# Performance work log

Measured on AMD Instinct MI355X. Metric: run time of the kernel, lower is better.

The kernel has to match this reference:

```python
import jax, jax.numpy as jnp
import numpy as np

N_NODES = 16000
N_EDGES = 256000
F = 128        # invariant edge feature dim
MUL = 64       # multiplicity of env/V irreps (mul_gcd)
HID = 128      # mlp_n_hidden
SQRT3 = float(np.sqrt(3.0))

# e3nn-style activation normalization constant for silu:
# c = sqrt(E_{z~N(0,1)}[silu(z)^2]), so silu(z)/c has unit second moment.
_z = np.linspace(-12.0, 12.0, 100001)
_pdf = np.exp(-0.5 * _z ** 2) / np.sqrt(2.0 * np.pi)
_silu = _z / (1.0 + np.exp(-_z))
SILU_C = float(np.sqrt(np.trapz(_silu ** 2 * _pdf, _z)))


def _nsilu(x):
    return jax.nn.silu(x) / SILU_C


def _lin(x, W):
    # e3nn 'path' gradient normalization: W ~ N(0,1), forward scaled by 1/sqrt(fan_in)
    return (x @ W) / jnp.sqrt(jnp.asarray(W.shape[0], x.dtype))


def setup_inputs() -> dict:
    key = jax.random.key(0)
    ks = jax.random.split(key, 11)
    inp = {
        'vectors': jax.random.normal(ks[0], (N_EDGES, 3), jnp.float32),
        'x': jax.random.normal(ks[1], (N_EDGES, F), jnp.float32),
        'V': jax.random.normal(ks[2], (N_EDGES, 4 * MUL), jnp.float32),  # 64x0e + 64x1o
        'u': jax.random.uniform(ks[3], (N_EDGES,), jnp.float32),
        'm': jnp.ones((N_EDGES,), jnp.float32),
        'W_env': jax.random.normal(ks[4], (F, 2 * MUL), jnp.float32),
        'W1': jax.random.normal(ks[5], (F + 2 * MUL, HID), jnp.float32),
        'W2': jax.random.normal(ks[6], (HID, HID), jnp.float32),
        'W3': jax.random.normal(ks[7], (HID, HID), jnp.float32),
        'W_out': jax.random.normal(ks[8], (2 * MUL, MUL), jnp.float32),
        'senders': jax.random.randint(ks[9], (N_EDGES,), 0, N_NODES, jnp.int32),
    }
    return inp


def reference(vectors, x, V, u, m, W_env, W1, W2, W3, W_out, senders):
    E = vectors.shape[0]
    x = x * m[:, None]

    # n_neighbors = scatter_sum(m, dst=senders, map_back=True)
    n_neighbors = jax.ops.segment_sum(m, senders, num_segments=N_NODES)[senders]  # (E,)

    # w = Linear(num_irreps=2*MUL)(x)
    w = _lin(x, W_env)                  # (E, 128)
    w0, w1 = w[:, :MUL], w[:, MUL:]     # scalar / vector channel weights

    # spherical harmonics (component normalization): Y0 = 1, Y1 = sqrt(3)*rhat
    rhat = vectors / jnp.linalg.norm(vectors, axis=-1, keepdims=True)
    Y1 = SQRT3 * rhat                   # (E, 3)

    # w * Y * m, scatter_sum over senders, map back, normalize by n_neighbors
    denom = n_neighbors + 1e-5
    ws = w0 * m[:, None]                                   # (E, MUL)   w * Y0
    wv = (w1[:, :, None] * Y1[:, None, :]) * m[:, None, None]  # (E, MUL, 3)
    wY_s = jax.ops.segment_sum(ws, senders, num_segments=N_NODES)[senders] / denom[:, None]
    wY_v = jax.ops.segment_sum(wv, senders, num_segments=N_NODES)[senders] / denom[:, None, None]

    # V.mul_to_axis(): (E, MUL, 0e+1o)
    Vs = V[:, :MUL]                      # (E, MUL)
    Vv = V[:, MUL:].reshape(E, MUL, 3)   # (E, MUL, 3)

    # tensor product, filter_ir_out = {0e, 1o} (CG, component normalization)
    s_a = wY_s * Vs                                  # 0e x 0e -> 0e
    s_b = jnp.sum(wY_v * Vv, axis=-1) / SQRT3        # 1o x 1o -> 0e
    v_a = wY_s[:, :, None] * Vv                      # 0e x 1o -> 1o
    v_b = wY_v * Vs[:, :, None]                      # 1o x 0e -> 1o

    # scalars -> concatenated into x; vectors stay equivariant
    x = jnp.concatenate([x, s_a, s_b], axis=1)       # (E, F + 2*MUL)

    # invariant MLP (silu, no output activation)
    h = _nsilu(_lin(x, W1))
    h = _nsilu(_lin(h, W2))
    h = _lin(h, W3)                                  # (E, HID)
    x_out = u[:, None] * h

    # Linear(irreps_out=64x1o) on 128x1o
    V_in = jnp.concatenate([v_a, v_b], axis=1)       # (E, 2*MUL, 3)
    V_out = jnp.einsum('euk,uo->eok', V_in, W_out) / jnp.sqrt(jnp.asarray(2 * MUL, V.dtype))
    V_out = V_out.reshape(E, MUL * 3)                # (E, 192)

    return x_out, V_out
```

## Files before the change

kernel.cpp:

```cpp
#include <hip/hip_runtime.h>
#include <math.h>

typedef short bf16x8 __attribute__((ext_vector_type(8)));
typedef float f32x4 __attribute__((ext_vector_type(4)));

#define S128 0.08838834764831845f
#define S256I 0.0625f
#define NN_NODES 16000

#define WS_COUNTS   16448000
#define WS_OFFSETS  (WS_COUNTS + 64000)
#define WS_CURSOR   (WS_OFFSETS + 64000)
#define WS_ORDER    (WS_CURSOR + 64000)
#define WS_W1 (WS_ORDER + 1024000)
#define WS_W2 (WS_W1 + 65536)
#define WS_W3 (WS_W2 + 32768)
#define WS_WO (WS_W3 + 32768)
#define WS_WE (WS_WO + 16384)

static float compute_inv_silu_c() {
    double sum = 0.0, prev = 0.0;
    const double dz = 24.0 / 100000.0;
    for (int i = 0; i <= 100000; ++i) {
        double z = -12.0 + dz * (double)i;
        double pdf = exp(-0.5 * z * z) * 0.3989422804014327;
        double s = z / (1.0 + exp(-z));
        double f = s * s * pdf;
        if (i) sum += 0.5 * (prev + f) * dz;
        prev = f;
    }
    return (float)(1.0 / sqrt(sum));
}
static const float INV_SILU_C = compute_inv_silu_c();

__device__ __forceinline__ unsigned int packbf(float a, float b) {
    union { float f; unsigned int u; } ca, cb;
    ca.f = a; cb.f = b;
    unsigned int ua = ca.u + (0x7fffu + ((ca.u >> 16) & 1u));
    unsigned int ub = cb.u + (0x7fffu + ((cb.u >> 16) & 1u));
    return (ua >> 16) | (ub & 0xffff0000u);
}
__device__ __forceinline__ unsigned short bf16r(float v) {
    union { float f; unsigned int u; } c; c.f = v;
    return (unsigned short)((c.u + (0x7fffu + ((c.u >> 16) & 1u))) >> 16);
}
__device__ __forceinline__ float bflo(unsigned int u) { return __uint_as_float(u << 16); }
__device__ __forceinline__ float bfhi(unsigned int u) { return __uint_as_float(u & 0xffff0000u); }
__device__ __forceinline__ int swz(int row, int b) { return b ^ ((row & 7) << 4); }
__device__ __forceinline__ float nsilu(float v, float ic) {
    return v / (1.0f + __expf(-v)) * ic;
}

__global__ __launch_bounds__(256) void k_wprep(
    const float* __restrict__ W1, const float* __restrict__ W2,
    const float* __restrict__ W3, const float* __restrict__ Wout,
    const float* __restrict__ Wenv, char* __restrict__ wsb)
{
    const int t = blockIdx.x * 256 + threadIdx.x;
    if (t < NN_NODES) ((int*)(wsb + WS_COUNTS))[t] = 0;
    if (t < 32768) {
        int n = t & 127, k = t >> 7;
        *(unsigned short*)(wsb + WS_W1 + n * 512 + k * 2) =
            bf16r(W1[k * 128 + n] * S256I);
    }
    if (t < 16384) {
        int n = t & 127, k = t >> 7;
        *(unsigned short*)(wsb + WS_W2 + n * 256 + k * 2) =
            bf16r(W2[k * 128 + n] * S128);
        *(unsigned short*)(wsb + WS_W3 + n * 256 + k * 2) =
            bf16r(W3[k * 128 + n] * S128);
    }
    if (t < 16384) {
        int j = t & 127, k = t >> 7;
        int c = (j & 1) ? 64 + (j >> 1) : (j >> 1);
        *(unsigned short*)(wsb + WS_WE + j * 256 + ((k * 2) ^ ((j & 7) << 4))) =
            bf16r(Wenv[k * 128 + c] * S128);
    }
    if (t < 8192) {
        int o = t & 63, uu = t >> 6;
        *(unsigned short*)(wsb + WS_WO + o * 256 + ((uu * 2) ^ ((o & 7) << 4))) =
            bf16r(Wout[uu * 64 + o] * S128);
    }
}

__global__ __launch_bounds__(1024) void k_hist(
    const int* __restrict__ senders, int* __restrict__ counts, int E)
{
    const int e = blockIdx.x * 1024 + threadIdx.x;
    if (e < E) atomicAdd(&counts[senders[e]], 1);
}

__global__ __launch_bounds__(1024) void k_scan(
    const int* __restrict__ counts, int* __restrict__ offsets,
    int* __restrict__ cursor)
{
    __shared__ int part[1024];
    const int t = threadIdx.x;
    const int s0 = t * 16;
    const int s1 = (s0 + 16 < NN_NODES) ? s0 + 16 : NN_NODES;
    int s = 0;
    for (int i = s0; i < s1; ++i) s += counts[i];
    part[t] = s;
    __syncthreads();
    for (int off = 1; off < 1024; off <<= 1) {
        int v = part[t];
        if (t >= off) v += part[t - off];
        __syncthreads();
        part[t] = v;
        __syncthreads();
    }
    int run = t ? part[t - 1] : 0;
    for (int i = s0; i < s1; ++i) {
        offsets[i] = run; cursor[i] = run; run += counts[i];
    }
}

__global__ __launch_bounds__(1024) void k_binfill(
    const int* __restrict__ senders, int* __restrict__ cursor,
    int* __restrict__ order, int E)
{
    const int e = blockIdx.x * 1024 + threadIdx.x;
    if (e < E) {
        const int p = atomicAdd(&cursor[senders[e]], 1);
        order[p] = e;
    }
}

__global__ __launch_bounds__(512) void k_env(
    const float* __restrict__ x, const float* __restrict__ m,
    const char* __restrict__ wsb, char* __restrict__ wout, int E)
{
    __shared__ char lds[65536];
    const int tid = threadIdx.x;

    {
        const int4* src = (const int4*)(wsb + WS_WE);
        int4* dst = (int4*)(lds + 32768);
        #pragma unroll
        for (int j = 0; j < 4; ++j) dst[tid * 4 + j] = src[tid * 4 + j];
    }

    const int eb = blockIdx.x * 128;
    {
        const int el = tid >> 2, q = tid & 3;
        const int e = eb + el;
        if (e < E) {
            const float mv = m[e];
            const float4* xp = (const float4*)&x[(size_t)e * 128 + q * 32];
            #pragma unroll
            for (int j = 0; j < 4; ++j) {
                float4 A = xp[2 * j], B = xp[2 * j + 1];
                int4 w;
                w.x = packbf(A.x * mv, A.y * mv); w.y = packbf(A.z * mv, A.w * mv);
                w.z = packbf(B.x * mv, B.y * mv); w.w = packbf(B.z * mv, B.w * mv);
                *(int4*)(lds + el * 256 + swz(el, q * 64 + j * 16)) = w;
            }
        } else {
            const int4 z = {0, 0, 0, 0};
            #pragma unroll
            for (int j = 0; j < 4; ++j)
                *(int4*)(lds + el * 256 + swz(el, q * 64 + j * 16)) = z;
        }
    }
    __syncthreads();

    const int l = tid & 63, wid = tid >> 6;
    const int wm = wid & 3, wn = wid >> 2;
    const int m0 = wm * 32, n0 = wn * 64;
    const int lr = l & 15, lg = l >> 4;

    f32x4 acc[2][4];
    #pragma unroll
    for (int a = 0; a < 2; ++a)
        #pragma unroll
        for (int b = 0; b < 4; ++b) acc[a][b] = (f32x4){0.f, 0.f, 0.f, 0.f};

    #pragma unroll
    for (int kk = 0; kk < 4; ++kk) {
        const int kb = kk * 64 + lg * 16;
        bf16x8 a0 = *(const bf16x8*)(lds + (m0 + lr) * 256      + swz(m0 + lr, kb));
        bf16x8 a1 = *(const bf16x8*)(lds + (m0 + 16 + lr) * 256 + swz(m0 + 16 + lr, kb));
        #pragma unroll
        for (int nt = 0; nt < 4; ++nt) {
            const int row = n0 + nt * 16 + lr;
            bf16x8 bb = *(const bf16x8*)(lds + 32768 + row * 256 + swz(row, kb));
            acc[0][nt] = __builtin_amdgcn_mfma_f32_16x16x32_bf16(a0, bb, acc[0][nt], 0, 0, 0);
            acc[1][nt] = __builtin_amdgcn_mfma_f32_16x16x32_bf16(a1, bb, acc[1][nt], 0, 0, 0);
        }
    }
    __syncthreads();

    #pragma unroll
    for (int mt = 0; mt < 2; ++mt)
        #pragma unroll
        for (int nt = 0; nt < 4; ++nt)
            #pragma unroll
            for (int r = 0; r < 4; ++r) {
                const int row = m0 + mt * 16 + lg * 4 + r;
                const int col = n0 + nt * 16 + lr;
                *(unsigned short*)(lds + row * 256 + col * 2) = bf16r(acc[mt][nt][r]);
            }
    __syncthreads();
    {
        const int4* s = (const int4*)lds;
        int4* d = (int4*)(wout + (size_t)eb * 256);
        #pragma unroll
        for (int j = 0; j < 4; ++j) d[tid * 4 + j] = s[tid * 4 + j];
    }
}

__global__ __launch_bounds__(256) void k_gather(
    const char* __restrict__ wvb, const float* __restrict__ vectors,
    const float* __restrict__ m, const int* __restrict__ counts,
    const int* __restrict__ offsets, const int* __restrict__ order,
    float* __restrict__ node_cnt, float* __restrict__ node_s,
    float* __restrict__ node_v)
{
    const int l = threadIdx.x & 63, wid = threadIdx.x >> 6;
    const int n = blockIdx.x * 4 + wid;
    if (n >= NN_NODES) return;
    const int cnt = counts[n], base = offsets[n];

    float as = 0.f, a0 = 0.f, a1 = 0.f, a2 = 0.f, am = 0.f;
    for (int i = 0; i < cnt; ++i) {
        const int e = order[base + i];
        const unsigned int wv = *(const unsigned int*)(wvb + (size_t)e * 256 + l * 4);
        const float mm = m[e];
        const float vx = vectors[(size_t)e * 3 + 0];
        const float vy = vectors[(size_t)e * 3 + 1];
        const float vz = vectors[(size_t)e * 3 + 2];
        const float rn = 1.7320508075688772f / sqrtf(vx * vx + vy * vy + vz * vz);
        const float w0 = bflo(wv) * mm;
        const float c1 = bfhi(wv) * mm * rn;
        as += w0; am += mm;
        a0 += c1 * vx; a1 += c1 * vy; a2 += c1 * vz;
    }
    if (l == 0) node_cnt[n] = am;
    node_s[(size_t)n * 64 + l] = as;
    float* nv = &node_v[((size_t)n * 64 + l) * 3];
    nv[0] = a0; nv[1] = a1; nv[2] = a2;
}

__global__ __launch_bounds__(512) void k_prep_vout(
    const float* __restrict__ V, const int* __restrict__ senders,
    const float* __restrict__ node_cnt, const float* __restrict__ node_s,
    const float* __restrict__ node_v, const char* __restrict__ wsb,
    float* __restrict__ out_x, float* __restrict__ out_v, int E)
{
    __shared__ char lds[49152 + 16384];
    const int tid = threadIdx.x, l = tid & 63, wid = tid >> 6;

    {
        const int4* src = (const int4*)(wsb + WS_WO);
        int4 a = src[tid * 2], b = src[tid * 2 + 1];
        ((int4*)(lds + 49152))[tid * 2]     = a;
        ((int4*)(lds + 49152))[tid * 2 + 1] = b;
    }

    const int eb = blockIdx.x * 64;
    #pragma unroll 2
    for (int i = 0; i < 8; ++i) {
        const int el = wid * 8 + i;
        const int e  = eb + el;
        float Vs = 0.f, Vv0 = 0.f, Vv1 = 0.f, Vv2 = 0.f;
        float wYs = 0.f, wv0 = 0.f, wv1 = 0.f, wv2 = 0.f;
        if (e < E) {
            Vs = V[(size_t)e * 256 + l];
            const float* vp = &V[(size_t)e * 256 + 64 + l * 3];
            Vv0 = vp[0]; Vv1 = vp[1]; Vv2 = vp[2];
            const int sn = senders[e];
            const float rden = 1.0f / (node_cnt[sn] + 1e-5f);
            wYs = node_s[(size_t)sn * 64 + l] * rden;
            const float* nvp = &node_v[((size_t)sn * 64 + l) * 3];
            wv0 = nvp[0] * rden; wv1 = nvp[1] * rden; wv2 = nvp[2] * rden;
            unsigned short* sab = (unsigned short*)((char*)out_x + (size_t)e * 512);
            sab[l]      = bf16r(wYs * Vs);
            sab[64 + l] = bf16r((wv0 * Vv0 + wv1 * Vv1 + wv2 * Vv2) * 0.57735026918962576f);
        }
        const float vvk[3] = {Vv0, Vv1, Vv2};
        const float wvk[3] = {wv0, wv1, wv2};
        #pragma unroll
        for (int k = 0; k < 3; ++k) {
            const int row = el * 3 + k;
            *(unsigned short*)(lds + row * 256 + swz(row, l * 2))       = bf16r(wYs * vvk[k]);
            *(unsigned short*)(lds + row * 256 + swz(row, 128 + l * 2)) = bf16r(wvk[k] * Vs);
        }
    }
    __syncthreads();

    const int wm = wid & 3, wn = wid >> 2;
    const int m0 = wm * 48, n0 = wn * 32;
    const int lr = l & 15, lg = l >> 4;
    f32x4 acc[3][2];
    #pragma unroll
    for (int a = 0; a < 3; ++a)
        #pragma unroll
        for (int b = 0; b < 2; ++b) acc[a][b] = (f32x4){0.f, 0.f, 0.f, 0.f};

    #pragma unroll
    for (int kk = 0; kk < 4; ++kk) {
        const int kb = kk * 64 + lg * 16;
        bf16x8 a0 = *(const bf16x8*)(lds + (m0 + lr) * 256      + swz(m0 + lr, kb));
        bf16x8 a1 = *(const bf16x8*)(lds + (m0 + 16 + lr) * 256 + swz(m0 + 16 + lr, kb));
        bf16x8 a2 = *(const bf16x8*)(lds + (m0 + 32 + lr) * 256 + swz(m0 + 32 + lr, kb));
        bf16x8 b0 = *(const bf16x8*)(lds + 49152 + (n0 + lr) * 256      + swz(n0 + lr, kb));
        bf16x8 b1 = *(const bf16x8*)(lds + 49152 + (n0 + 16 + lr) * 256 + swz(n0 + 16 + lr, kb));
        acc[0][0] = __builtin_amdgcn_mfma_f32_16x16x32_bf16(a0, b0, acc[0][0], 0, 0, 0);
        acc[0][1] = __builtin_amdgcn_mfma_f32_16x16x32_bf16(a0, b1, acc[0][1], 0, 0, 0);
        acc[1][0] = __builtin_amdgcn_mfma_f32_16x16x32_bf16(a1, b0, acc[1][0], 0, 0, 0);
        acc[1][1] = __builtin_amdgcn_mfma_f32_16x16x32_bf16(a1, b1, acc[1][1], 0, 0, 0);
        acc[2][0] = __builtin_amdgcn_mfma_f32_16x16x32_bf16(a2, b0, acc[2][0], 0, 0, 0);
        acc[2][1] = __builtin_amdgcn_mfma_f32_16x16x32_bf16(a2, b1, acc[2][1], 0, 0, 0);
    }
    __syncthreads();

    #pragma unroll
    for (int mt = 0; mt < 3; ++mt)
        #pragma unroll
        for (int nt = 0; nt < 2; ++nt)
            #pragma unroll
            for (int r = 0; r < 4; ++r) {
                const int mm = m0 + mt * 16 + lg * 4 + r;
                const int el2 = mm / 3, kd = mm - el2 * 3;
                const int o = n0 + nt * 16 + lr;
                *(float*)(lds + el2 * 768 + (o * 3 + kd) * 4) = acc[mt][nt][r];
            }
    __syncthreads();
    if (eb + 64 <= E) {
        const int4* s = (const int4*)lds;
        int4* d = (int4*)(out_v + (size_t)eb * 192);
        #pragma unroll
        for (int j = 0; j < 6; ++j) d[tid * 6 + j] = s[tid * 6 + j];
    } else {
        for (int idx = tid; idx < 64 * 192; idx += 512) {
            const int el2 = idx / 192;
            if (eb + el2 < E)
                out_v[(size_t)(eb + el2) * 192 + (idx % 192)] = *(float*)(lds + idx * 4);
        }
    }
}

__global__ __launch_bounds__(512, 4) void k_mlp(
    const float* __restrict__ x, const float* __restrict__ m,
    const float* __restrict__ ug, const char* __restrict__ wsb,
    float* __restrict__ out_x, float inv_c, int E)
{
    __shared__ char lds[65536];
    const int tid = threadIdx.x;

    const int eb = blockIdx.x * 128;
    {
        const int el = tid >> 2, q = tid & 3;
        const int e  = eb + el;
        if (e < E) {
            const float mv = m[e];
            const float4* xp = (const float4*)&x[(size_t)e * 128 + q * 32];
            #pragma unroll
            for (int j = 0; j < 4; ++j) {
                float4 A = xp[2 * j], B = xp[2 * j + 1];
                int4 w;
                w.x = packbf(A.x * mv, A.y * mv); w.y = packbf(A.z * mv, A.w * mv);
                w.z = packbf(B.x * mv, B.y * mv); w.w = packbf(B.z * mv, B.w * mv);
                *(int4*)(lds + el * 512 + swz(el, q * 64 + j * 16)) = w;
            }
            const int4* sp = (const int4*)((const char*)out_x + (size_t)e * 512 + q * 64);
            #pragma unroll
            for (int j = 0; j < 4; ++j) {
                int4 v = sp[j];
                *(int4*)(lds + el * 512 + swz(el, 256 + q * 64 + j * 16)) = v;
            }
        } else {
            const int4 z = {0, 0, 0, 0};
            #pragma unroll
            for (int j = 0; j < 4; ++j) {
                *(int4*)(lds + el * 512 + swz(el, q * 64 + j * 16)) = z;
                *(int4*)(lds + el * 512 + swz(el, 256 + q * 64 + j * 16)) = z;
            }
        }
    }
    __syncthreads();

    const int l = tid & 63, wid = tid >> 6;
    const int wm = wid >> 1, wn = wid & 1;
    const int m0 = wm * 32, n0 = wn * 64;
    const int lr = l & 15, lg = l >> 4;

    const char* w1g = wsb + WS_W1;
    const char* w2g = wsb + WS_W2;
    const char* w3g = wsb + WS_W3;

    f32x4 acc[2][4];
    #pragma unroll
    for (int a = 0; a < 2; ++a)
        #pragma unroll
        for (int b = 0; b < 4; ++b) acc[a][b] = (f32x4){0.f, 0.f, 0.f, 0.f};
    #pragma unroll 2
    for (int kk = 0; kk < 8; ++kk) {
        const int kb = kk * 64 + lg * 16;
        bf16x8 a0 = *(const bf16x8*)(lds + (m0 + lr) * 512      + swz(m0 + lr, kb));
        bf16x8 a1 = *(const bf16x8*)(lds + (m0 + 16 + lr) * 512 + swz(m0 + 16 + lr, kb));
        #pragma unroll
        for (int nt = 0; nt < 4; ++nt) {
            const int row = n0 + nt * 16 + lr;
            bf16x8 bb = *(const bf16x8*)(w1g + row * 512 + kb);
            acc[0][nt] = __builtin_amdgcn_mfma_f32_16x16x32_bf16(a0, bb, acc[0][nt], 0, 0, 0);
            acc[1][nt] = __builtin_amdgcn_mfma_f32_16x16x32_bf16(a1, bb, acc[1][nt], 0, 0, 0);
        }
    }
    __syncthreads();

    #pragma unroll
    for (int mt = 0; mt < 2; ++mt)
        #pragma unroll
        for (int nt = 0; nt < 4; ++nt)
            #pragma unroll
            for (int r = 0; r < 4; ++r) {
                const int row = m0 + mt * 16 + lg * 4 + r;
                const int col = n0 + nt * 16 + lr;
                *(unsigned short*)(lds + row * 256 + swz(row, col * 2)) =
                    bf16r(nsilu(acc[mt][nt][r], inv_c));
            }
    __syncthreads();

    f32x4 acc2[2][4];
    #pragma unroll
    for (int a = 0; a < 2; ++a)
        #pragma unroll
        for (int b = 0; b < 4; ++b) acc2[a][b] = (f32x4){0.f, 0.f, 0.f, 0.f};
    #pragma unroll
    for (int kk = 0; kk < 4; ++kk) {
        const int kb = kk * 64 + lg * 16;
        bf16x8 a0 = *(const bf16x8*)(lds + (m0 + lr) * 256      + swz(m0 + lr, kb));
        bf16x8 a1 = *(const bf16x8*)(lds + (m0 + 16 + lr) * 256 + swz(m0 + 16 + lr, kb));
        #pragma unroll
        for (int nt = 0; nt < 4; ++nt) {
            const int row = n0 + nt * 16 + lr;
            bf16x8 bb = *(const bf16x8*)(w2g + row * 256 + kb);
            acc2[0][nt] = __builtin_amdgcn_mfma_f32_16x16x32_bf16(a0, bb, acc2[0][nt], 0, 0, 0);
            acc2[1][nt] = __builtin_amdgcn_mfma_f32_16x16x32_bf16(a1, bb, acc2[1][nt], 0, 0, 0);
        }
    }
    #pragma unroll
    for (int mt = 0; mt < 2; ++mt)
        #pragma unroll
        for (int nt = 0; nt < 4; ++nt)
            #pragma unroll
            for (int r = 0; r < 4; ++r) {
                const int row = m0 + mt * 16 + lg * 4 + r;
                const int col = n0 + nt * 16 + lr;
                *(unsigned short*)(lds + 32768 + row * 256 + swz(row, col * 2)) =
                    bf16r(nsilu(acc2[mt][nt][r], inv_c));
            }
    __syncthreads();

    f32x4 acc3[2][4];
    #pragma unroll
    for (int a = 0; a < 2; ++a)
        #pragma unroll
        for (int b = 0; b < 4; ++b) acc3[a][b] = (f32x4){0.f, 0.f, 0.f, 0.f};
    #pragma unroll
    for (int kk = 0; kk < 4; ++kk) {
        const int kb = kk * 64 + lg * 16;
        bf16x8 a0 = *(const bf16x8*)(lds + 32768 + (m0 + lr) * 256      + swz(m0 + lr, kb));
        bf16x8 a1 = *(const bf16x8*)(lds + 32768 + (m0 + 16 + lr) * 256 + swz(m0 + 16 + lr, kb));
        #pragma unroll
        for (int nt = 0; nt < 4; ++nt) {
            const int row = n0 + nt * 16 + lr;
            bf16x8 bb = *(const bf16x8*)(w3g + row * 256 + kb);
            acc3[0][nt] = __builtin_amdgcn_mfma_f32_16x16x32_bf16(a0, bb, acc3[0][nt], 0, 0, 0);
            acc3[1][nt] = __builtin_amdgcn_mfma_f32_16x16x32_bf16(a1, bb, acc3[1][nt], 0, 0, 0);
        }
    }
    #pragma unroll
    for (int mt = 0; mt < 2; ++mt)
        #pragma unroll
        for (int r = 0; r < 4; ++r) {
            const int e = eb + m0 + mt * 16 + lg * 4 + r;
            if (e < E) {
                const float uu = ug[e];
                #pragma unroll
                for (int nt = 0; nt < 4; ++nt)
                    out_x[(size_t)e * 128 + n0 + nt * 16 + lr] = uu * acc3[mt][nt][r];
            }
        }
}

extern "C" void kernel_launch(void* const* d_in, const int* in_sizes, int n_in,
                              void* d_out, int out_size, void* d_ws, size_t ws_size,
                              hipStream_t stream) {
    const float* vectors = (const float*)d_in[0];
    const float* x       = (const float*)d_in[1];
    const float* V       = (const float*)d_in[2];
    const float* u       = (const float*)d_in[3];
    const float* m       = (const float*)d_in[4];
    const float* W_env   = (const float*)d_in[5];
    const float* W1      = (const float*)d_in[6];
    const float* W2      = (const float*)d_in[7];
    const float* W3      = (const float*)d_in[8];
    const float* W_out   = (const float*)d_in[9];
    const int*   senders = (const int*)d_in[10];

    const int E = in_sizes[4];

    char*  wsb      = (char*)d_ws;
    float* node_cnt = (float*)d_ws;
    float* node_s   = node_cnt + NN_NODES;
    float* node_v   = node_s + (size_t)NN_NODES * 64;
    int* counts  = (int*)(wsb + WS_COUNTS);
    int* offsets = (int*)(wsb + WS_OFFSETS);
    int* cursor  = (int*)(wsb + WS_CURSOR);
    int* order   = (int*)(wsb + WS_ORDER);

    float* out_x = (float*)d_out;
    float* out_v = out_x + (size_t)E * 128;
    char*  wvb   = (char*)out_v;

    k_wprep<<<128, 256, 0, stream>>>(W1, W2, W3, W_out, W_env, wsb);
    k_hist<<<(E + 1023) / 1024, 1024, 0, stream>>>(senders, counts, E);
    k_scan<<<1, 1024, 0, stream>>>(counts, offsets, cursor);
    k_binfill<<<(E + 1023) / 1024, 1024, 0, stream>>>(senders, cursor, order, E);
    k_env<<<(E + 127) / 128, 512, 0, stream>>>(x, m, wsb, wvb, E);
    k_gather<<<(NN_NODES + 3) / 4, 256, 0, stream>>>(wvb, vectors, m, counts,
                                                     offsets, order,
                                                     node_cnt, node_s, node_v);
    k_prep_vout<<<(E + 63) / 64, 512, 0, stream>>>(V, senders, node_cnt, node_s,
                                                   node_v, wsb, out_x, out_v, E);
    k_mlp<<<(E + 127) / 128, 512, 0, stream>>>(x, m, u, wsb, out_x, INV_SILU_C, E);
}
```

Baseline: 507.4 us.

## Hold weight fragments in registers and stage outputs through LDS in env and MLP kernels

```diff
diff --git a/kernel.cpp b/kernel.cpp
--- a/kernel.cpp
+++ b/kernel.cpp
@@ -73,7 +73,7 @@
     if (t < 16384) {
         int j = t & 127, k = t >> 7;
         int c = (j & 1) ? 64 + (j >> 1) : (j >> 1);
-        *(unsigned short*)(wsb + WS_WE + j * 256 + ((k * 2) ^ ((j & 7) << 4))) =
+        *(unsigned short*)(wsb + WS_WE + j * 256 + k * 2) =
             bf16r(Wenv[k * 128 + c] * S128);
     }
     if (t < 8192) {
@@ -130,15 +130,15 @@
     const float* __restrict__ x, const float* __restrict__ m,
     const char* __restrict__ wsb, char* __restrict__ wout, int E)
 {
-    __shared__ char lds[65536];
-    const int tid = threadIdx.x;
-
-    {
-        const int4* src = (const int4*)(wsb + WS_WE);
-        int4* dst = (int4*)(lds + 32768);
-        #pragma unroll
-        for (int j = 0; j < 4; ++j) dst[tid * 4 + j] = src[tid * 4 + j];
-    }
+    __shared__ char lds[32768];
+    const int tid = threadIdx.x, l = tid & 63, wid = tid >> 6;
+    const int lr = l & 15, lg = l >> 4;
+    const int n0 = wid * 16;
+
+    bf16x8 B[4];
+    #pragma unroll
+    for (int kk = 0; kk < 4; ++kk)
+        B[kk] = *(const bf16x8*)(wsb + WS_WE + (n0 + lr) * 256 + kk * 64 + lg * 16);
 
     const int eb = blockIdx.x * 128;
     {
@@ -149,10 +149,10 @@
             const float4* xp = (const float4*)&x[(size_t)e * 128 + q * 32];
             #pragma unroll
             for (int j = 0; j < 4; ++j) {
-                float4 A = xp[2 * j], B = xp[2 * j + 1];
+                float4 A = xp[2 * j], Bv = xp[2 * j + 1];
                 int4 w;
                 w.x = packbf(A.x * mv, A.y * mv); w.y = packbf(A.z * mv, A.w * mv);
-                w.z = packbf(B.x * mv, B.y * mv); w.w = packbf(B.z * mv, B.w * mv);
+                w.z = packbf(Bv.x * mv, Bv.y * mv); w.w = packbf(Bv.z * mv, Bv.w * mv);
                 *(int4*)(lds + el * 256 + swz(el, q * 64 + j * 16)) = w;
             }
         } else {
@@ -164,48 +164,41 @@
     }
     __syncthreads();
 
-    const int l = tid & 63, wid = tid >> 6;
-    const int wm = wid & 3, wn = wid >> 2;
-    const int m0 = wm * 32, n0 = wn * 64;
-    const int lr = l & 15, lg = l >> 4;
-
-    f32x4 acc[2][4];
-    #pragma unroll
-    for (int a = 0; a < 2; ++a)
-        #pragma unroll
-        for (int b = 0; b < 4; ++b) acc[a][b] = (f32x4){0.f, 0.f, 0.f, 0.f};
+    f32x4 acc[8];
+    #pragma unroll
+    for (int a = 0; a < 8; ++a) acc[a] = (f32x4){0.f, 0.f, 0.f, 0.f};
 
     #pragma unroll
     for (int kk = 0; kk < 4; ++kk) {
         const int kb = kk * 64 + lg * 16;
-        bf16x8 a0 = *(const bf16x8*)(lds + (m0 + lr) * 256      + swz(m0 + lr, kb));
-        bf16x8 a1 = *(const bf16x8*)(lds + (m0 + 16 + lr) * 256 + swz(m0 + 16 + lr, kb));
-        #pragma unroll
-        for (int nt = 0; nt < 4; ++nt) {
-            const int row = n0 + nt * 16 + lr;
-            bf16x8 bb = *(const bf16x8*)(lds + 32768 + row * 256 + swz(row, kb));
-            acc[0][nt] = __builtin_amdgcn_mfma_f32_16x16x32_bf16(a0, bb, acc[0][nt], 0, 0, 0);
-            acc[1][nt] = __builtin_amdgcn_mfma_f32_16x16x32_bf16(a1, bb, acc[1][nt], 0, 0, 0);
-        }
-    }
-    __syncthreads();
-
-    #pragma unroll
-    for (int mt = 0; mt < 2; ++mt)
-        #pragma unroll
-        for (int nt = 0; nt < 4; ++nt)
+        #pragma unroll
+        for (int mt = 0; mt < 8; ++mt) {
+            const int row = mt * 16 + lr;
+            bf16x8 a = *(const bf16x8*)(lds + row * 256 + swz(row, kb));
+            acc[mt] = __builtin_amdgcn_mfma_f32_16x16x32_bf16(a, B[kk], acc[mt], 0, 0, 0);
+        }
+    }
+    __syncthreads();
+
+    #pragma unroll
+    for (int mt = 0; mt < 8; ++mt)
+        #pragma unroll
+        for (int r = 0; r < 4; ++r) {
+            const int row = mt * 16 + lg * 4 + r;
+            *(unsigned short*)(lds + row * 256 + (((n0 + lr) * 2) ^ ((row & 7) << 4))) =
+                bf16r(acc[mt][r]);
+        }
+    __syncthreads();
+
+    {
+        const int el = tid >> 2, q = tid & 3;
+        const int e = eb + el;
+        if (e < E) {
+            int4* d = (int4*)(wout + (size_t)e * 256 + q * 64);
             #pragma unroll
-            for (int r = 0; r < 4; ++r) {
-                const int row = m0 + mt * 16 + lg * 4 + r;
-                const int col = n0 + nt * 16 + lr;
-                *(unsigned short*)(lds + row * 256 + col * 2) = bf16r(acc[mt][nt][r]);
-            }
-    __syncthreads();
-    {
-        const int4* s = (const int4*)lds;
-        int4* d = (int4*)(wout + (size_t)eb * 256);
-        #pragma unroll
-        for (int j = 0; j < 4; ++j) d[tid * 4 + j] = s[tid * 4 + j];
+            for (int j = 0; j < 4; ++j)
+                d[j] = *(int4*)(lds + el * 256 + ((q * 64 + j * 16) ^ ((el & 7) << 4)));
+        }
     }
 }
 
@@ -345,144 +338,137 @@
     const float* __restrict__ ug, const char* __restrict__ wsb,
     float* __restrict__ out_x, float inv_c, int E)
 {
-    __shared__ char lds[65536];
-    const int tid = threadIdx.x;
-
-    const int eb = blockIdx.x * 128;
+    __shared__ char lds[49152];
+    const int tid = threadIdx.x, l = tid & 63, wid = tid >> 6;
+    const int lr = l & 15, lg = l >> 4;
+    const int n0 = wid * 16;
+    const int eb = blockIdx.x * 64;
+
+    bf16x8 B1[8];
+    #pragma unroll
+    for (int kk = 0; kk < 8; ++kk)
+        B1[kk] = *(const bf16x8*)(wsb + WS_W1 + (n0 + lr) * 512 + kk * 64 + lg * 16);
+
     {
-        const int el = tid >> 2, q = tid & 3;
-        const int e  = eb + el;
+        const int el = tid >> 3, q = tid & 7;
+        const int e = eb + el;
         if (e < E) {
             const float mv = m[e];
-            const float4* xp = (const float4*)&x[(size_t)e * 128 + q * 32];
+            const float4* xp = (const float4*)&x[(size_t)e * 128 + q * 16];
+            float4 A = xp[0], Bv = xp[1], C = xp[2], D = xp[3];
+            int4 w0, w1;
+            w0.x = packbf(A.x * mv, A.y * mv);   w0.y = packbf(A.z * mv, A.w * mv);
+            w0.z = packbf(Bv.x * mv, Bv.y * mv); w0.w = packbf(Bv.z * mv, Bv.w * mv);
+            w1.x = packbf(C.x * mv, C.y * mv);   w1.y = packbf(C.z * mv, C.w * mv);
+            w1.z = packbf(D.x * mv, D.y * mv);   w1.w = packbf(D.z * mv, D.w * mv);
+            *(int4*)(lds + el * 512 + swz(el, q * 32))      = w0;
+            *(int4*)(lds + el * 512 + swz(el, q * 32 + 16)) = w1;
+            const int4* sp = (const int4*)((const char*)out_x + (size_t)e * 512 + q * 32);
+            *(int4*)(lds + el * 512 + swz(el, 256 + q * 32))      = sp[0];
+            *(int4*)(lds + el * 512 + swz(el, 256 + q * 32 + 16)) = sp[1];
+        } else {
+            const int4 z = {0, 0, 0, 0};
+            *(int4*)(lds + el * 512 + swz(el, q * 32))            = z;
+            *(int4*)(lds + el * 512 + swz(el, q * 32 + 16))       = z;
+            *(int4*)(lds + el * 512 + swz(el, 256 + q * 32))      = z;
+            *(int4*)(lds + el * 512 + swz(el, 256 + q * 32 + 16)) = z;
+        }
+    }
+    __syncthreads();
+
+    f32x4 a1[4];
+    #pragma unroll
+    for (int a = 0; a < 4; ++a) a1[a] = (f32x4){0.f, 0.f, 0.f, 0.f};
+    #pragma unroll
+    for (int kk = 0; kk < 8; ++kk) {
+        const int kb = kk * 64 + lg * 16;
+        #pragma unroll
+        for (int mt = 0; mt < 4; ++mt) {
+            const int row = mt * 16 + lr;
+            bf16x8 a = *(const bf16x8*)(lds + row * 512 + swz(row, kb));
+            a1[mt] = __builtin_amdgcn_mfma_f32_16x16x32_bf16(a, B1[kk], a1[mt], 0, 0, 0);
+        }
+    }
+
+    bf16x8 B2[4], B3[4];
+    #pragma unroll
+    for (int kk = 0; kk < 4; ++kk) {
+        B2[kk] = *(const bf16x8*)(wsb + WS_W2 + (n0 + lr) * 256 + kk * 64 + lg * 16);
+        B3[kk] = *(const bf16x8*)(wsb + WS_W3 + (n0 + lr) * 256 + kk * 64 + lg * 16);
+    }
+
+    #pragma unroll
+    for (int mt = 0; mt < 4; ++mt)
+        #pragma unroll
+        for (int r = 0; r < 4; ++r) {
+            const int row = mt * 16 + lg * 4 + r;
+            *(unsigned short*)(lds + 32768 + row * 256 + swz(row, (n0 + lr) * 2)) =
+                bf16r(nsilu(a1[mt][r], inv_c));
+        }
+    __syncthreads();
+
+    f32x4 a2[4];
+    #pragma unroll
+    for (int a = 0; a < 4; ++a) a2[a] = (f32x4){0.f, 0.f, 0.f, 0.f};
+    #pragma unroll
+    for (int kk = 0; kk < 4; ++kk) {
+        const int kb = kk * 64 + lg * 16;
+        #pragma unroll
+        for (int mt = 0; mt < 4; ++mt) {
+            const int row = mt * 16 + lr;
+            bf16x8 a = *(const bf16x8*)(lds + 32768 + row * 256 + swz(row, kb));
+            a2[mt] = __builtin_amdgcn_mfma_f32_16x16x32_bf16(a, B2[kk], a2[mt], 0, 0, 0);
+        }
+    }
+    #pragma unroll
+    for (int mt = 0; mt < 4; ++mt)
+        #pragma unroll
+        for (int r = 0; r < 4; ++r) {
+            const int row = mt * 16 + lg * 4 + r;
+            *(unsigned short*)(lds + row * 256 + swz(row, (n0 + lr) * 2)) =
+                bf16r(nsilu(a2[mt][r], inv_c));
+        }
+    __syncthreads();
+
+    f32x4 a3[4];
+    #pragma unroll
+    for (int a = 0; a < 4; ++a) a3[a] = (f32x4){0.f, 0.f, 0.f, 0.f};
+    #pragma unroll
+    for (int kk = 0; kk < 4; ++kk) {
+        const int kb = kk * 64 + lg * 16;
+        #pragma unroll
+        for (int mt = 0; mt < 4; ++mt) {
+            const int row = mt * 16 + lr;
+            bf16x8 a = *(const bf16x8*)(lds + row * 256 + swz(row, kb));
+            a3[mt] = __builtin_amdgcn_mfma_f32_16x16x32_bf16(a, B3[kk], a3[mt], 0, 0, 0);
+        }
+    }
+    __syncthreads();
+
+    #pragma unroll
+    for (int mt = 0; mt < 4; ++mt)
+        #pragma unroll
+        for (int r = 0; r < 4; ++r) {
+            const int row = mt * 16 + lg * 4 + r;
+            *(float*)(lds + row * 512 + (((n0 + lr) * 4) ^ ((row & 7) << 4))) = a3[mt][r];
+        }
+    __syncthreads();
+
+    {
+        const int el = tid >> 3, q = tid & 7;
+        const int e = eb + el;
+        if (e < E) {
+            const float uu = ug[e];
             #pragma unroll
             for (int j = 0; j < 4; ++j) {
-                float4 A = xp[2 * j], B = xp[2 * j + 1];
-                int4 w;
-                w.x = packbf(A.x * mv, A.y * mv); w.y = packbf(A.z * mv, A.w * mv);
-                w.z = packbf(B.x * mv, B.y * mv); w.w = packbf(B.z * mv, B.w * mv);
-                *(int4*)(lds + el * 512 + swz(el, q * 64 + j * 16)) = w;
+                int4 v = *(int4*)(lds + el * 512 + ((q * 64 + j * 16) ^ ((el & 7) << 4)));
+                float4 f;
+                f.x = __int_as_float(v.x) * uu; f.y = __int_as_float(v.y) * uu;
+                f.z = __int_as_float(v.z) * uu; f.w = __int_as_float(v.w) * uu;
+                *(float4*)(&out_x[(size_t)e * 128 + q * 16 + j * 4]) = f;
             }
-            const int4* sp = (const int4*)((const char*)out_x + (size_t)e * 512 + q * 64);
-            #pragma unroll
-            for (int j = 0; j < 4; ++j) {
-                int4 v = sp[j];
-                *(int4*)(lds + el * 512 + swz(el, 256 + q * 64 + j * 16)) = v;
-            }
-        } else {
-            const int4 z = {0, 0, 0, 0};
-            #pragma unroll
-            for (int j = 0; j < 4; ++j) {
-                *(int4*)(lds + el * 512 + swz(el, q * 64 + j * 16)) = z;
-                *(int4*)(lds + el * 512 + swz(el, 256 + q * 64 + j * 16)) = z;
-            }
-        }
-    }
-    __syncthreads();
-
-    const int l = tid & 63, wid = tid >> 6;
-    const int wm = wid >> 1, wn = wid & 1;
-    const int m0 = wm * 32, n0 = wn * 64;
-    const int lr = l & 15, lg = l >> 4;
-
-    const char* w1g = wsb + WS_W1;
-    const char* w2g = wsb + WS_W2;
-    const char* w3g = wsb + WS_W3;
-
-    f32x4 acc[2][4];
-    #pragma unroll
-    for (int a = 0; a < 2; ++a)
-        #pragma unroll
-        for (int b = 0; b < 4; ++b) acc[a][b] = (f32x4){0.f, 0.f, 0.f, 0.f};
-    #pragma unroll 2
-    for (int kk = 0; kk < 8; ++kk) {
-        const int kb = kk * 64 + lg * 16;
-        bf16x8 a0 = *(const bf16x8*)(lds + (m0 + lr) * 512      + swz(m0 + lr, kb));
-        bf16x8 a1 = *(const bf16x8*)(lds + (m0 + 16 + lr) * 512 + swz(m0 + 16 + lr, kb));
-        #pragma unroll
-        for (int nt = 0; nt < 4; ++nt) {
-            const int row = n0 + nt * 16 + lr;
-            bf16x8 bb = *(const bf16x8*)(w1g + row * 512 + kb);
-            acc[0][nt] = __builtin_amdgcn_mfma_f32_16x16x32_bf16(a0, bb, acc[0][nt], 0, 0, 0);
-            acc[1][nt] = __builtin_amdgcn_mfma_f32_16x16x32_bf16(a1, bb, acc[1][nt], 0, 0, 0);
-        }
-    }
-    __syncthreads();
-
-    #pragma unroll
-    for (int mt = 0; mt < 2; ++mt)
-        #pragma unroll
-        for (int nt = 0; nt < 4; ++nt)
-            #pragma unroll
-            for (int r = 0; r < 4; ++r) {
-                const int row = m0 + mt * 16 + lg * 4 + r;
-                const int col = n0 + nt * 16 + lr;
-                *(unsigned short*)(lds + row * 256 + swz(row, col * 2)) =
-                    bf16r(nsilu(acc[mt][nt][r], inv_c));
-            }
-    __syncthreads();
-
-    f32x4 acc2[2][4];
-    #pragma unroll
-    for (int a = 0; a < 2; ++a)
-        #pragma unroll
-        for (int b = 0; b < 4; ++b) acc2[a][b] = (f32x4){0.f, 0.f, 0.f, 0.f};
-    #pragma unroll
-    for (int kk = 0; kk < 4; ++kk) {
-        const int kb = kk * 64 + lg * 16;
-        bf16x8 a0 = *(const bf16x8*)(lds + (m0 + lr) * 256      + swz(m0 + lr, kb));
-        bf16x8 a1 = *(const bf16x8*)(lds + (m0 + 16 + lr) * 256 + swz(m0 + 16 + lr, kb));
-        #pragma unroll
-        for (int nt = 0; nt < 4; ++nt) {
-            const int row = n0 + nt * 16 + lr;
-            bf16x8 bb = *(const bf16x8*)(w2g + row * 256 + kb);
-            acc2[0][nt] = __builtin_amdgcn_mfma_f32_16x16x32_bf16(a0, bb, acc2[0][nt], 0, 0, 0);
-            acc2[1][nt] = __builtin_amdgcn_mfma_f32_16x16x32_bf16(a1, bb, acc2[1][nt], 0, 0, 0);
-        }
-    }
-    #pragma unroll
-    for (int mt = 0; mt < 2; ++mt)
-        #pragma unroll
-        for (int nt = 0; nt < 4; ++nt)
-            #pragma unroll
-            for (int r = 0; r < 4; ++r) {
-                const int row = m0 + mt * 16 + lg * 4 + r;
-                const int col = n0 + nt * 16 + lr;
-                *(unsigned short*)(lds + 32768 + row * 256 + swz(row, col * 2)) =
-                    bf16r(nsilu(acc2[mt][nt][r], inv_c));
-            }
-    __syncthreads();
-
-    f32x4 acc3[2][4];
-    #pragma unroll
-    for (int a = 0; a < 2; ++a)
-        #pragma unroll
-        for (int b = 0; b < 4; ++b) acc3[a][b] = (f32x4){0.f, 0.f, 0.f, 0.f};
-    #pragma unroll
-    for (int kk = 0; kk < 4; ++kk) {
-        const int kb = kk * 64 + lg * 16;
-        bf16x8 a0 = *(const bf16x8*)(lds + 32768 + (m0 + lr) * 256      + swz(m0 + lr, kb));
-        bf16x8 a1 = *(const bf16x8*)(lds + 32768 + (m0 + 16 + lr) * 256 + swz(m0 + 16 + lr, kb));
-        #pragma unroll
-        for (int nt = 0; nt < 4; ++nt) {
-            const int row = n0 + nt * 16 + lr;
-            bf16x8 bb = *(const bf16x8*)(w3g + row * 256 + kb);
-            acc3[0][nt] = __builtin_amdgcn_mfma_f32_16x16x32_bf16(a0, bb, acc3[0][nt], 0, 0, 0);
-            acc3[1][nt] = __builtin_amdgcn_mfma_f32_16x16x32_bf16(a1, bb, acc3[1][nt], 0, 0, 0);
-        }
-    }
-    #pragma unroll
-    for (int mt = 0; mt < 2; ++mt)
-        #pragma unroll
-        for (int r = 0; r < 4; ++r) {
-            const int e = eb + m0 + mt * 16 + lg * 4 + r;
-            if (e < E) {
-                const float uu = ug[e];
-                #pragma unroll
-                for (int nt = 0; nt < 4; ++nt)
-                    out_x[(size_t)e * 128 + n0 + nt * 16 + lr] = uu * acc3[mt][nt][r];
-            }
-        }
+        }
+    }
 }
 
 extern "C" void kernel_launch(void* const* d_in, const int* in_sizes, int n_in,
@@ -525,5 +511,5 @@
                                                      node_cnt, node_s, node_v);
     k_prep_vout<<<(E + 63) / 64, 512, 0, stream>>>(V, senders, node_cnt, node_s,
                                                    node_v, wsb, out_x, out_v, E);
-    k_mlp<<<(E + 127) / 128, 512, 0, stream>>>(x, m, u, wsb, out_x, INV_SILU_C, E);
-}
+    k_mlp<<<(E + 63) / 64, 512, 0, stream>>>(x, m, u, wsb, out_x, INV_SILU_C, E);
+}
```

Result: faster. 455.3 us (-10.3%).
